# Kernel optimization log

Measured on AMD Instinct MI355X. Metric: run time of the kernel, lower is better.

Reference implementation:

```python
import jax, jax.numpy as jnp
import numpy as np

B, L, T = 32, 256, 32
V_SIZE, D, H = 30000, 300, 256


def _gru(x, h0, Wih, Whh, bih, bhh):
    # x: [B,S,D], h0: [B,H]; PyTorch GRU gate order: r, z, n
    xg = jnp.einsum('bsd,gd->bsg', x, Wih) + bih  # [B,S,3H]

    def step(h, xg_t):
        gh = jnp.einsum('bh,gh->bg', h, Whh) + bhh
        ir, iz, in_ = jnp.split(xg_t, 3, axis=-1)
        hr, hz, hn_ = jnp.split(gh, 3, axis=-1)
        r = jax.nn.sigmoid(ir + hr)
        z = jax.nn.sigmoid(iz + hz)
        n = jnp.tanh(in_ + r * hn_)
        h_new = (1.0 - z) * n + z * h
        return h_new, h_new

    h_last, outs = jax.lax.scan(step, h0, jnp.swapaxes(xg, 0, 1))
    return jnp.swapaxes(outs, 0, 1), h_last  # [B,S,H], [B,H]


def setup_inputs() -> dict:
    rng = np.random.default_rng(0)
    Xin = rng.integers(0, V_SIZE, (B, L)).astype(np.int64)
    # strictly increasing segment ends; starts = previous end + 1
    Yindex = np.stack([np.sort(rng.choice(L, T, replace=False)) for _ in range(B)]).astype(np.int64)
    Xindex = np.concatenate([np.zeros((B, 1), np.int64), Yindex[:, :-1] + 1], axis=1)
    lens = np.full((B,), L, np.int64)
    s = 0.05
    p = lambda *shape: jnp.asarray(rng.standard_normal(shape) * s, jnp.float32)
    return {
        'Xin': jnp.asarray(Xin), 'Xindex': jnp.asarray(Xindex),
        'Yindex': jnp.asarray(Yindex), 'lens': jnp.asarray(lens),
        'emb': jnp.asarray(rng.standard_normal((V_SIZE, D)) * 0.1, jnp.float32),
        'Wih_e': p(3 * H, D), 'Whh_e': p(3 * H, H), 'bih_e': p(3 * H), 'bhh_e': p(3 * H),
        'Wih_d': p(3 * H, D), 'Whh_d': p(3 * H, H), 'bih_d': p(3 * H), 'bhh_d': p(3 * H),
        'W1': p(H, H), 'W2': p(H, H), 'Vv': p(H),
    }


def reference(Xin, Xindex, Yindex, lens, emb, Wih_e, Whh_e, bih_e, bhh_e,
              Wih_d, Whh_d, bih_d, bhh_d, W1, W2, Vv):
    # pointerEncoder (isbanor=False, dropout=0, lens==L so packed == plain)
    X = emb[Xin]                                   # [B,L,D]
    h0 = jnp.zeros((Xin.shape[0], Whh_e.shape[1]), X.dtype)
    hn, h_end = _gru(X, h0, Wih_e, Whh_e, bih_e, bhh_e)  # [B,L,H],[B,H]
    # training_decoder, vectorized over batch and decode steps
    dec_tok = jnp.take_along_axis(Xin, Xindex, axis=1)   # token ids at segment starts
    dx = emb[dec_tok]                              # [B,T,D]
    dout, _ = _gru(dx, h_end, Wih_d, Whh_d, bih_d, bhh_d)  # [B,T,H]
    # pointerLayer: v = selu(V . selu(W1 en + W2 d)), masked log_softmax over [start, curL)
    WE = jnp.einsum('blh,kh->blk', hn, W1)         # [B,L,H]
    WD = jnp.einsum('bth,kh->btk', dout, W2)       # [B,T,H]
    s = jax.nn.selu(WE[:, None, :, :] + WD[:, :, None, :])  # [B,T,L,H]
    v = jax.nn.selu(jnp.einsum('btlh,h->btl', s, Vv))        # [B,T,L]
    pos = jnp.arange(hn.shape[1])
    mask = (pos[None, None, :] >= Xindex[:, :, None]) & (pos[None, None, :] < lens[:, None, None])
    logits = jnp.where(mask, v, -jnp.inf)
    logp = jax.nn.log_softmax(logits, axis=-1)
    tgt_logp = jnp.take_along_axis(logp, Yindex[:, :, None], axis=-1)[..., 0]  # [B,T]
    return -jnp.mean(tgt_logp)  # batch_loss / LoopN
```

## Files before the change

### kernel.cpp

```cpp
#include <hip/hip_runtime.h>
#include <hip/hip_bf16.h>
#include <stdint.h>

#define B_  32
#define L_  256
#define T_  32
#define D_  300
#define H_  256
#define G3  768

__device__ __forceinline__ int sdot4(uint32_t a, uint32_t b, int acc) {
#if defined(__has_builtin) && __has_builtin(__builtin_amdgcn_sdot4)
  return __builtin_amdgcn_sdot4((int)a, (int)b, acc, false);
#else
  const int a0 = (int)(signed char)(a & 0xff),  b0 = (int)(signed char)(b & 0xff);
  const int a1 = (int)(signed char)((a >> 8) & 0xff),  b1 = (int)(signed char)((b >> 8) & 0xff);
  const int a2 = (int)(signed char)((a >> 16) & 0xff), b2 = (int)(signed char)((b >> 16) & 0xff);
  const int a3 = (int)(signed char)(a >> 24),          b3 = (int)(signed char)(b >> 24);
  return acc + a0 * b0 + a1 * b1 + a2 * b2 + a3 * b3;
#endif
}

__device__ __forceinline__ int sdot8(uint32_t a, uint32_t b, int acc) {
#if defined(__has_builtin) && __has_builtin(__builtin_amdgcn_sdot8)
  return __builtin_amdgcn_sdot8((int)a, (int)b, acc, false);
#else
  const uint32_t M = 0xF0F0F0F0u;
  const uint32_t alo = (a << 4) & M, ahi = a & M;
  const uint32_t blo = (b << 4) & M, bhi = b & M;
  return acc + ((sdot4(alo, blo, 0) + sdot4(ahi, bhi, 0)) >> 8);
#endif
}

__device__ __forceinline__ float rcp_f(float x) { return __builtin_amdgcn_rcpf(x); }
__device__ __forceinline__ float sigmoid_f(float x) { return rcp_f(1.0f + __expf(-x)); }
__device__ __forceinline__ float tanh_f(float x) {
  float e2 = __expf(2.0f * x);
  return 1.0f - 2.0f * rcp_f(e2 + 1.0f);
}
__device__ __forceinline__ uint16_t f2bf(float x) {
  uint32_t u = __builtin_bit_cast(uint32_t, x);
  return (uint16_t)((u + 0x7FFF + ((u >> 16) & 1)) >> 16);
}
__device__ __forceinline__ float bf2f(uint16_t b) {
  uint32_t u = ((uint32_t)b) << 16;
  return __builtin_bit_cast(float, u);
}

__device__ __forceinline__ void pack_body(int blk, const float* __restrict__ Whh,
                                          uint32_t* __restrict__ wQ,
                                          float* __restrict__ sw) {
  const int row = blk * 4 + (threadIdx.x >> 6);
  const int lane = threadIdx.x & 63;
  const float* wr = Whh + (long)row * H_;
  float m = 0.0f;
#pragma unroll
  for (int u = 0; u < 4; ++u) m = fmaxf(m, fabsf(wr[lane + 64 * u]));
  for (int off = 32; off > 0; off >>= 1) m = fmaxf(m, __shfl_xor(m, off, 64));
  const float inv = m > 0.0f ? 7.0f / m : 0.0f;
  if (lane == 0) sw[row] = m > 0.0f ? m / 49.0f : 0.0f;
  if (lane < 32) {
    const int pd = lane;
    uint32_t d = 0;
#pragma unroll
    for (int jn = 0; jn < 8; ++jn) {
      int v = __float2int_rn(wr[8 * pd + jn] * inv);
      v = v > 7 ? 7 : (v < -7 ? -7 : v);
      d |= ((uint32_t)(v & 0xF)) << (4 * jn);
    }
    wQ[(((size_t)(pd >> 2) * G3 + row) << 2) + (pd & 3)] = d;
  }
}

__device__ __forceinline__ void quant_body(int blk, const float* __restrict__ A,
                                           const int* __restrict__ rowidx,
                                           const int* __restrict__ Xin2,
                                           const int* __restrict__ Xidx2,
                                           uint32_t* __restrict__ out,
                                           float* __restrict__ scale,
                                           int M, int K, int Kd) {
  const int row = blk * 4 + (threadIdx.x >> 6);
  const int lane = threadIdx.x & 63;
  if (row >= M) return;
  long src = row;
  if (rowidx) src = rowidx[row];
  else if (Xin2) src = Xin2[(row >> 5) * L_ + Xidx2[row]];
  const float* ar = A + src * (long)K;
  float m = 0.0f;
  for (int e = lane; e < K; e += 64) m = fmaxf(m, fabsf(ar[e]));
  for (int off = 32; off > 0; off >>= 1) m = fmaxf(m, __shfl_xor(m, off, 64));
  const float inv = m > 0.0f ? 127.0f / m : 0.0f;
  if (lane == 0) scale[row] = m * (1.0f / 127.0f);
  for (int kd = lane; kd < Kd; kd += 64) {
    uint32_t d = 0;
#pragma unroll
    for (int u = 0; u < 4; ++u) {
      const int e = 4 * kd + u;
      int qv = (e < K) ? __float2int_rn(ar[e] * inv) : 0;
      qv = qv > 127 ? 127 : (qv < -127 ? -127 : qv);
      d |= ((uint32_t)(qv & 0xff)) << (8 * u);
    }
    out[(long)row * Kd + kd] = d;
  }
}

__device__ __forceinline__ void quant16(int blk, const float* __restrict__ A,
                                        uint32_t* __restrict__ out,
                                        float* __restrict__ scale,
                                        int M, int K, int Kd) {
  const int row = blk * 16 + (threadIdx.x >> 6);
  const int lane = threadIdx.x & 63;
  if (row >= M) return;
  const float* ar = A + (long)row * K;
  float m = 0.0f;
  for (int e = lane; e < K; e += 64) m = fmaxf(m, fabsf(ar[e]));
  for (int off = 32; off > 0; off >>= 1) m = fmaxf(m, __shfl_xor(m, off, 64));
  const float inv = m > 0.0f ? 127.0f / m : 0.0f;
  if (lane == 0) scale[row] = m * (1.0f / 127.0f);
  for (int kd = lane; kd < Kd; kd += 64) {
    uint32_t d = 0;
#pragma unroll
    for (int u = 0; u < 4; ++u) {
      const int e = 4 * kd + u;
      int qv = (e < K) ? __float2int_rn(ar[e] * inv) : 0;
      qv = qv > 127 ? 127 : (qv < -127 ? -127 : qv);
      d |= ((uint32_t)(qv & 0xff)) << (8 * u);
    }
    out[(long)row * Kd + kd] = d;
  }
}

__global__ __launch_bounds__(256)
void prep_all(const float* __restrict__ Whh_e, const float* __restrict__ Whh_d,
              uint32_t* __restrict__ wQ_e, uint32_t* __restrict__ wQ_d,
              float* __restrict__ sw_e, float* __restrict__ sw_d,
              const float* __restrict__ Wih_e, const float* __restrict__ Wih_d,
              uint32_t* __restrict__ WihQ_e, uint32_t* __restrict__ WihQ_d,
              float* __restrict__ sWih_e, float* __restrict__ sWih_d,
              const float* __restrict__ W1, const float* __restrict__ W2,
              uint32_t* __restrict__ W1q, uint32_t* __restrict__ W2q,
              float* __restrict__ sW1, float* __restrict__ sW2,
              const float* __restrict__ emb, const int* __restrict__ Xin,
              const int* __restrict__ Xindex,
              uint32_t* __restrict__ Aqe, float* __restrict__ saAe,
              uint32_t* __restrict__ Aqd, float* __restrict__ saAd,
              const float* __restrict__ bih_e, const float* __restrict__ bhh_e,
              float* __restrict__ bsum_e,
              const float* __restrict__ bih_d, const float* __restrict__ bhh_d,
              float* __restrict__ bsum_d) {
  const int blk = blockIdx.x;
  if (blk < 192)        pack_body(blk, Whh_e, wQ_e, sw_e);
  else if (blk < 384)   pack_body(blk - 192, Whh_d, wQ_d, sw_d);
  else if (blk < 576)   quant_body(blk - 384, Wih_e, nullptr, nullptr, nullptr,
                                   WihQ_e, sWih_e, 768, 300, 80);
  else if (blk < 768)   quant_body(blk - 576, Wih_d, nullptr, nullptr, nullptr,
                                   WihQ_d, sWih_d, 768, 300, 80);
  else if (blk < 832)   quant_body(blk - 768, W1, nullptr, nullptr, nullptr,
                                   W1q, sW1, 256, 256, 64);
  else if (blk < 896)   quant_body(blk - 832, W2, nullptr, nullptr, nullptr,
                                   W2q, sW2, 256, 256, 64);
  else if (blk < 2944)  quant_body(blk - 896, emb, Xin, nullptr, nullptr,
                                   Aqe, saAe, 8192, 300, 80);
  else if (blk < 3200)  quant_body(blk - 2944, emb, nullptr, Xin, Xindex,
                                   Aqd, saAd, 1024, 300, 80);
  else {
    const int blk2 = blk - 3200;
    const int i = (blk2 % 3) * 256 + threadIdx.x;
    const float* bih = blk2 < 3 ? bih_e : bih_d;
    const float* bhh = blk2 < 3 ? bhh_e : bhh_d;
    float* bsum = blk2 < 3 ? bsum_e : bsum_d;
    float v = bih[i];
    if (i < 2 * H_) v += bhh[i];
    bsum[i] = v;
  }
}

__device__ __forceinline__
void gemm_body(const uint32_t* __restrict__ Aq, const float* __restrict__ sa,
               const uint32_t* __restrict__ Wq, const float* __restrict__ swc,
               const float* __restrict__ bias, void* __restrict__ C,
               int bm, int bn, int M, int N, int Kd,
               bool transp, bool biasF, bool bf16out) {
  __shared__ uint32_t As[8][68];
  __shared__ uint32_t Ws[8][68];
  const int tid = threadIdx.x;
  const int ty = tid >> 4, tx = tid & 15;
  const int srow = tid >> 2;
  const int skd = (tid & 3) << 1;
  const uint32_t* Arow = Aq + (long)(bm * 64 + srow) * Kd + skd;
  const uint32_t* Wrow = Wq + (long)(bn * 64 + srow) * Kd + skd;
  int acc[4][4] = {};
  for (int k0 = 0; k0 < Kd; k0 += 8) {
    const uint32_t a0 = Arow[k0], a1 = Arow[k0 + 1];
    const uint32_t w0 = Wrow[k0], w1 = Wrow[k0 + 1];
    __syncthreads();
    As[skd][srow] = a0; As[skd + 1][srow] = a1;
    Ws[skd][srow] = w0; Ws[skd + 1][srow] = w1;
    __syncthreads();
#pragma unroll
    for (int kd = 0; kd < 8; ++kd) {
      const uint4 a4 = *(const uint4*)&As[kd][ty << 2];
      const uint4 b4 = *(const uint4*)&Ws[kd][tx << 2];
      acc[0][0] = sdot4(a4.x, b4.x, acc[0][0]);
      acc[0][1] = sdot4(a4.x, b4.y, acc[0][1]);
      acc[0][2] = sdot4(a4.x, b4.z, acc[0][2]);
      acc[0][3] = sdot4(a4.x, b4.w, acc[0][3]);
      acc[1][0] = sdot4(a4.y, b4.x, acc[1][0]);
      acc[1][1] = sdot4(a4.y, b4.y, acc[1][1]);
      acc[1][2] = sdot4(a4.y, b4.z, acc[1][2]);
      acc[1][3] = sdot4(a4.y, b4.w, acc[1][3]);
      acc[2][0] = sdot4(a4.z, b4.x, acc[2][0]);
      acc[2][1] = sdot4(a4.z, b4.y, acc[2][1]);
      acc[2][2] = sdot4(a4.z, b4.z, acc[2][2]);
      acc[2][3] = sdot4(a4.z, b4.w, acc[2][3]);
      acc[3][0] = sdot4(a4.w, b4.x, acc[3][0]);
      acc[3][1] = sdot4(a4.w, b4.y, acc[3][1]);
      acc[3][2] = sdot4(a4.w, b4.z, acc[3][2]);
      acc[3][3] = sdot4(a4.w, b4.w, acc[3][3]);
    }
  }
#pragma unroll
  for (int i = 0; i < 4; ++i) {
    const int m = bm * 64 + (ty << 2) + i;
    const float sai = sa[m];
#pragma unroll
    for (int j = 0; j < 4; ++j) {
      const int n = bn * 64 + (tx << 2) + j;
      float v = (float)acc[i][j] * sai * swc[n];
      if (biasF) v += bias[n];
      const long idx = transp ? ((((long)(m >> 8) * N + n) << 8) + (m & 255))
                              : ((long)m * N + n);
      if (bf16out) ((uint16_t*)C)[idx] = f2bf(v);
      else         ((float*)C)[idx] = v;
    }
  }
}

__global__ __launch_bounds__(256)
void xg_gemms(const uint32_t* __restrict__ Aqe, const float* __restrict__ saAe,
              const uint32_t* __restrict__ WihQ_e, const float* __restrict__ sWih_e,
              const float* __restrict__ bsum_e, uint16_t* __restrict__ xg_e,
              const uint32_t* __restrict__ Aqd, const float* __restrict__ saAd,
              const uint32_t* __restrict__ WihQ_d, const float* __restrict__ sWih_d,
              const float* __restrict__ bsum_d, uint16_t* __restrict__ xg_d) {
  const int blk = blockIdx.x;
  if (blk < 1536)
    gemm_body(Aqe, saAe, WihQ_e, sWih_e, bsum_e, xg_e,
              blk % 128, blk / 128, 8192, 768, 80, false, true, true);
  else {
    const int k = blk - 1536;
    gemm_body(Aqd, saAd, WihQ_d, sWih_d, bsum_d, xg_d,
              k % 16, k / 16, 1024, 768, 80, false, true, true);
  }
}


#define PIN4(v) asm volatile("" : "+v"(v.x), "+v"(v.y), "+v"(v.z), "+v"(v.w))
#define DOT8V(acc, p_, h_) { \
  acc = sdot8(p_.x, h_.x, acc); acc = sdot8(p_.y, h_.y, acc); \
  acc = sdot8(p_.z, h_.z, acc); acc = sdot8(p_.w, h_.w, acc); }

#define LGKM_BARRIER() { \
  asm volatile("s_waitcnt lgkmcnt(0)" ::: "memory"); \
  __builtin_amdgcn_s_barrier(); }

__device__ __forceinline__
void gru_block(int b, const uint16_t* __restrict__ xg, const uint4* __restrict__ wQv,
               const float* __restrict__ sw, const float* __restrict__ bhh,
               const float* __restrict__ h0, float* __restrict__ hout,
               float* __restrict__ hlast, int S,
               uint32_t (*h2)[32], int4 (*partv)[H_]) {
  const int tid = threadIdx.x;
  const int j = tid & 255;
  const int q = tid >> 8;
  const uint4* wp = wQv + (q * 2) * G3 + j;
  uint4 wr0 = wp[0],      wr1 = wp[G3];
  uint4 wz0 = wp[H_],     wz1 = wp[G3 + H_];
  uint4 wn0 = wp[2 * H_], wn1 = wp[G3 + 2 * H_];
  PIN4(wr0); PIN4(wr1); PIN4(wz0); PIN4(wz1); PIN4(wn0); PIN4(wn1);
  float bhn = 0.0f, h = 0.0f, swr = 0.0f, swz = 0.0f, swn = 0.0f;
  const uint16_t* xp = xg + (long)b * S * G3;
  float* hp_out = hout + (long)b * S * H_;
  if (q == 0) {
    bhn = bhh[2 * H_ + j];
    swr = sw[j]; swz = sw[H_ + j]; swn = sw[2 * H_ + j];
    h = h0 ? h0[b * H_ + j] : 0.0f;
    int hq4 = __float2int_rn(h * 7.0f);
    hq4 = hq4 > 7 ? 7 : (hq4 < -7 ? -7 : hq4);
    const int hq4n = __shfl_down(hq4, 1, 64);
    if (!(j & 1))
      ((uint8_t*)h2[0])[j >> 1] = (uint8_t)((hq4 & 0xF) | ((hq4n & 0xF) << 4));
  }
  __syncthreads();
  for (int t = 0; t < S; ++t) {
    const uint4* hq = (const uint4*)h2[t & 1] + q * 2;
    const uint4 ha = hq[0], hb = hq[1];
    float xr = 0.0f, xz = 0.0f, xn = 0.0f;
    if (q == 0) {
      xr = bf2f(xp[j]); xz = bf2f(xp[H_ + j]); xn = bf2f(xp[2 * H_ + j]);
    }
    int ar = 0, az = 0, an = 0;
    DOT8V(ar, wr0, ha) DOT8V(ar, wr1, hb)
    DOT8V(az, wz0, ha) DOT8V(az, wz1, hb)
    DOT8V(an, wn0, ha) DOT8V(an, wn1, hb)
    if (q) partv[q][j] = make_int4(ar, az, an, 0);
    LGKM_BARRIER();
    if (q == 0) {
      const int4 p1 = partv[1][j];
      const int4 p2 = partv[2][j];
      const int4 p3 = partv[3][j];
      const float arf = (float)(ar + p1.x + p2.x + p3.x) * swr;
      const float azf = (float)(az + p1.y + p2.y + p3.y) * swz;
      const float anf = (float)(an + p1.z + p2.z + p3.z) * swn;
      const float r = sigmoid_f(xr + arf);
      const float z = sigmoid_f(xz + azf);
      const float n = tanh_f(xn + r * (anf + bhn));
      h = (1.0f - z) * n + z * h;
      hp_out[j] = h;
      int hq4 = __float2int_rn(h * 7.0f);
      hq4 = hq4 > 7 ? 7 : (hq4 < -7 ? -7 : hq4);
      const int hq4n = __shfl_down(hq4, 1, 64);
      if (!(j & 1))
        ((uint8_t*)h2[(t & 1) ^ 1])[j >> 1] =
            (uint8_t)((hq4 & 0xF) | ((hq4n & 0xF) << 4));
    }
    xp += G3;
    hp_out += H_;
    LGKM_BARRIER();
  }
  if (q == 0 && hlast) hlast[b * H_ + j] = h;
}

__global__ __launch_bounds__(1024)
void gru_enc(const uint16_t* __restrict__ xg, const uint4* __restrict__ wQv,
             const float* __restrict__ sw, const float* __restrict__ bhh,
             float* __restrict__ hout, float* __restrict__ hlast, int S) {
  __shared__ __align__(16) uint32_t h2[2][32];
  __shared__ int4 partv[4][H_];
  gru_block(blockIdx.x, xg, wQv, sw, bhh, nullptr, hout, hlast, S, h2, partv);
}

__global__ __launch_bounds__(1024)
void dec_and_hquant(const uint16_t* __restrict__ xg_d, const uint4* __restrict__ wQ_d,
                    const float* __restrict__ sw_d, const float* __restrict__ bhh_d,
                    const float* __restrict__ hend, float* __restrict__ doutb,
                    const float* __restrict__ hn, uint32_t* __restrict__ hnq,
                    float* __restrict__ sahn) {
  __shared__ __align__(16) uint32_t h2[2][32];
  __shared__ int4 partv[4][H_];
  if (blockIdx.x < 32)
    gru_block(blockIdx.x, xg_d, wQ_d, sw_d, bhh_d, hend, doutb,
              (float*)nullptr, T_, h2, partv);
  else
    quant16(blockIdx.x - 32, hn, hnq, sahn, 8192, 256, 64);
}

__global__ __launch_bounds__(256)
void wet_and_dquant(const uint32_t* __restrict__ hnq, const float* __restrict__ sahn,
                    const uint32_t* __restrict__ W1q, const float* __restrict__ sW1,
                    float* __restrict__ WEt,
                    const float* __restrict__ doutb, uint32_t* __restrict__ dq,
                    float* __restrict__ sad) {
  if (blockIdx.x < 512)
    gemm_body(hnq, sahn, W1q, sW1, nullptr, WEt,
              blockIdx.x & 127, blockIdx.x >> 7, 8192, 256, 64, true, false, false);
  else
    quant_body(blockIdx.x - 512, doutb, nullptr, nullptr, nullptr,
               dq, sad, 1024, 256, 64);
}

__global__ __launch_bounds__(256)
void wd_gemm(const uint32_t* __restrict__ dq, const float* __restrict__ sad,
             const uint32_t* __restrict__ W2q, const float* __restrict__ sW2,
             float* __restrict__ WDb) {
  gemm_body(dq, sad, W2q, sW2, nullptr, WDb,
            blockIdx.x & 15, blockIdx.x >> 4, 1024, 256, 64, false, false, false);
}

__global__ __launch_bounds__(256)
void pointer_loss(const float* __restrict__ WEt, const float* __restrict__ WD,
                  const float* __restrict__ Vv,
                  const int* __restrict__ Xindex, const int* __restrict__ Yindex,
                  const int* __restrict__ lens, float* __restrict__ out) {
  const int t = blockIdx.x, b = blockIdx.y;
  const int l = threadIdx.x;
  __shared__ float wd_s[H_], vv_s[H_];
  __shared__ float rbuf[4], sbuf[4], vy_s;
  const int bt = b * T_ + t;
  wd_s[l] = WD[(long)bt * H_ + l];
  vv_s[l] = Vv[l] * 1.0507009873554805f;
  __syncthreads();
  const float* wet = WEt + (long)b * H_ * L_;
  const float alpha = 1.6732632423543772f;
  float acc = 0.0f;
#pragma unroll 4
  for (int hh = 0; hh < H_; ++hh) {
    const float xsum = wet[hh * L_ + l] + wd_s[hh];
    const float sneg = alpha * (__expf(xsum) - 1.0f);
    const float s = xsum > 0.0f ? xsum : sneg;
    acc = fmaf(s, vv_s[hh], acc);
  }
  float v;
  {
    const float sneg = alpha * (__expf(acc) - 1.0f);
    v = 1.0507009873554805f * (acc > 0.0f ? acc : sneg);
  }
  const int start = Xindex[bt];
  const int len = lens[b];
  const bool valid = (l >= start) && (l < len);
  const int y = Yindex[bt];
  if (l == y) vy_s = v;
  float m = valid ? v : -INFINITY;
  for (int off = 32; off > 0; off >>= 1) m = fmaxf(m, __shfl_xor(m, off, 64));
  const int wid = l >> 6, lane = l & 63;
  if (lane == 0) rbuf[wid] = m;
  __syncthreads();
  const float mx = fmaxf(fmaxf(rbuf[0], rbuf[1]), fmaxf(rbuf[2], rbuf[3]));
  float e = valid ? __expf(v - mx) : 0.0f;
  for (int off = 32; off > 0; off >>= 1) e += __shfl_xor(e, off, 64);
  if (lane == 0) sbuf[wid] = e;
  __syncthreads();
  if (l == 0) {
    const float sum = sbuf[0] + sbuf[1] + sbuf[2] + sbuf[3];
    atomicAdd(out, (mx + __logf(sum) - vy_s) * (1.0f / (B_ * T_)));
  }
}

extern "C" void kernel_launch(void* const* d_in, const int* in_sizes, int n_in,
                              void* d_out, int out_size, void* d_ws, size_t ws_size,
                              hipStream_t stream) {
  (void)in_sizes; (void)n_in; (void)out_size; (void)ws_size;
  const int*   Xin    = (const int*)d_in[0];
  const int*   Xindex = (const int*)d_in[1];
  const int*   Yindex = (const int*)d_in[2];
  const int*   lens   = (const int*)d_in[3];
  const float* emb    = (const float*)d_in[4];
  const float* Wih_e  = (const float*)d_in[5];
  const float* Whh_e  = (const float*)d_in[6];
  const float* bih_e  = (const float*)d_in[7];
  const float* bhh_e  = (const float*)d_in[8];
  const float* Wih_d  = (const float*)d_in[9];
  const float* Whh_d  = (const float*)d_in[10];
  const float* bih_d  = (const float*)d_in[11];
  const float* bhh_d  = (const float*)d_in[12];
  const float* W1     = (const float*)d_in[13];
  const float* W2     = (const float*)d_in[14];
  const float* Vv     = (const float*)d_in[15];

  char* p = (char*)d_ws;
  auto take = [&](size_t bytes) { void* q = (void*)p; p += (bytes + 255) & ~(size_t)255; return q; };
  uint32_t* wQ_e   = (uint32_t*)take((size_t)32 * G3 * 4);
  uint32_t* wQ_d   = (uint32_t*)take((size_t)32 * G3 * 4);
  float*    sw_e   = (float*)take((size_t)768 * 4);
  float*    sw_d   = (float*)take((size_t)768 * 4);
  uint32_t* WihQ_e = (uint32_t*)take((size_t)768 * 80 * 4);
  uint32_t* WihQ_d = (uint32_t*)take((size_t)768 * 80 * 4);
  float*    sWih_e = (float*)take((size_t)768 * 4);
  float*    sWih_d = (float*)take((size_t)768 * 4);
  uint32_t* W1q    = (uint32_t*)take((size_t)256 * 64 * 4);
  uint32_t* W2q    = (uint32_t*)take((size_t)256 * 64 * 4);
  float*    sW1    = (float*)take((size_t)256 * 4);
  float*    sW2    = (float*)take((size_t)256 * 4);
  float*    bsum_e = (float*)take((size_t)768 * 4);
  float*    bsum_d = (float*)take((size_t)768 * 4);
  uint16_t* xg_e   = (uint16_t*)take((size_t)8192 * 768 * 2);
  uint16_t* xg_d   = (uint16_t*)take((size_t)1024 * 768 * 2);
  float*    hn     = (float*)take((size_t)8192 * 256 * 4);
  float*    hend   = (float*)take((size_t)8192 * 4);
  float*    doutb  = (float*)take((size_t)1024 * 256 * 4);
  float*    WDb    = (float*)take((size_t)1024 * 256 * 4);
  float*    WEt    = (float*)take((size_t)8192 * 256 * 4);
  uint32_t* Aqe    = (uint32_t*)take((size_t)8192 * 80 * 4);
  float*    saAe   = (float*)take((size_t)8192 * 4);
  uint32_t* Aqd    = (uint32_t*)take((size_t)1024 * 80 * 4);
  float*    saAd   = (float*)take((size_t)1024 * 4);
  uint32_t* hnq  = Aqe;
  float*    sahn = saAe;
  uint32_t* dq   = Aqd;
  float*    sad  = saAd;

  hipMemsetAsync(d_out, 0, sizeof(float), stream);

  hipLaunchKernelGGL(prep_all, dim3(3206), dim3(256), 0, stream,
                     Whh_e, Whh_d, wQ_e, wQ_d, sw_e, sw_d,
                     Wih_e, Wih_d, WihQ_e, WihQ_d, sWih_e, sWih_d,
                     W1, W2, W1q, W2q, sW1, sW2,
                     emb, Xin, Xindex, Aqe, saAe, Aqd, saAd,
                     bih_e, bhh_e, bsum_e, bih_d, bhh_d, bsum_d);

  hipLaunchKernelGGL(xg_gemms, dim3(1728), dim3(256), 0, stream,
                     Aqe, saAe, WihQ_e, sWih_e, bsum_e, xg_e,
                     Aqd, saAd, WihQ_d, sWih_d, bsum_d, xg_d);

  hipLaunchKernelGGL(gru_enc, dim3(32), dim3(1024), 0, stream,
                     xg_e, (const uint4*)wQ_e, sw_e, bhh_e, hn, hend, L_);

  hipLaunchKernelGGL(dec_and_hquant, dim3(544), dim3(1024), 0, stream,
                     xg_d, (const uint4*)wQ_d, sw_d, bhh_d, hend, doutb,
                     hn, hnq, sahn);

  hipLaunchKernelGGL(wet_and_dquant, dim3(768), dim3(256), 0, stream,
                     hnq, sahn, W1q, sW1, WEt, doutb, dq, sad);

  hipLaunchKernelGGL(wd_gemm, dim3(64), dim3(256), 0, stream,
                     dq, sad, W2q, sW2, WDb);

  hipLaunchKernelGGL(pointer_loss, dim3(T_, B_), dim3(256), 0, stream,
                     WEt, WDb, Vv, Xindex, Yindex, lens, (float*)d_out);
}
```

Before: 287.2 us.

## Run GRU recurrence with one thread per hidden unit, dropping cross-wave reduction

Each GRU block now uses 256 threads, and each thread holds the full recurrent weight row (96 uint4 registers) for its hidden unit. This removes the 4-way K split, the LDS partial-sum exchange and one barrier per timestep. It also prefetches the next step's input gates into registers so the global load overlaps the dot products. The cost is much higher register pressure and fewer waves per block to hide latency. The hn quantization blocks move to 4-row 256-thread blocks, which raises their grid count.

```diff
diff --git a/kernel.cpp b/kernel.cpp
--- a/kernel.cpp
+++ b/kernel.cpp
@@ -86,32 +86,6 @@
   if (rowidx) src = rowidx[row];
   else if (Xin2) src = Xin2[(row >> 5) * L_ + Xidx2[row]];
   const float* ar = A + src * (long)K;
-  float m = 0.0f;
-  for (int e = lane; e < K; e += 64) m = fmaxf(m, fabsf(ar[e]));
-  for (int off = 32; off > 0; off >>= 1) m = fmaxf(m, __shfl_xor(m, off, 64));
-  const float inv = m > 0.0f ? 127.0f / m : 0.0f;
-  if (lane == 0) scale[row] = m * (1.0f / 127.0f);
-  for (int kd = lane; kd < Kd; kd += 64) {
-    uint32_t d = 0;
-#pragma unroll
-    for (int u = 0; u < 4; ++u) {
-      const int e = 4 * kd + u;
-      int qv = (e < K) ? __float2int_rn(ar[e] * inv) : 0;
-      qv = qv > 127 ? 127 : (qv < -127 ? -127 : qv);
-      d |= ((uint32_t)(qv & 0xff)) << (8 * u);
-    }
-    out[(long)row * Kd + kd] = d;
-  }
-}
-
-__device__ __forceinline__ void quant16(int blk, const float* __restrict__ A,
-                                        uint32_t* __restrict__ out,
-                                        float* __restrict__ scale,
-                                        int M, int K, int Kd) {
-  const int row = blk * 16 + (threadIdx.x >> 6);
-  const int lane = threadIdx.x & 63;
-  if (row >= M) return;
-  const float* ar = A + (long)row * K;
   float m = 0.0f;
   for (int e = lane; e < K; e += 64) m = fmaxf(m, fabsf(ar[e]));
   for (int off = 32; off > 0; off >>= 1) m = fmaxf(m, __shfl_xor(m, off, 64));
@@ -264,95 +238,99 @@
   asm volatile("s_waitcnt lgkmcnt(0)" ::: "memory"); \
   __builtin_amdgcn_s_barrier(); }
 
+#define CHUNK(c) { \
+  const uint4 hc = hq[c]; \
+  DOT8V(ar, wr##c, hc) DOT8V(az, wz##c, hc) DOT8V(an, wn##c, hc) }
+
 __device__ __forceinline__
 void gru_block(int b, const uint16_t* __restrict__ xg, const uint4* __restrict__ wQv,
                const float* __restrict__ sw, const float* __restrict__ bhh,
                const float* __restrict__ h0, float* __restrict__ hout,
-               float* __restrict__ hlast, int S,
-               uint32_t (*h2)[32], int4 (*partv)[H_]) {
-  const int tid = threadIdx.x;
-  const int j = tid & 255;
-  const int q = tid >> 8;
-  const uint4* wp = wQv + (q * 2) * G3 + j;
-  uint4 wr0 = wp[0],      wr1 = wp[G3];
-  uint4 wz0 = wp[H_],     wz1 = wp[G3 + H_];
-  uint4 wn0 = wp[2 * H_], wn1 = wp[G3 + 2 * H_];
-  PIN4(wr0); PIN4(wr1); PIN4(wz0); PIN4(wz1); PIN4(wn0); PIN4(wn1);
-  float bhn = 0.0f, h = 0.0f, swr = 0.0f, swz = 0.0f, swn = 0.0f;
-  const uint16_t* xp = xg + (long)b * S * G3;
-  float* hp_out = hout + (long)b * S * H_;
-  if (q == 0) {
-    bhn = bhh[2 * H_ + j];
-    swr = sw[j]; swz = sw[H_ + j]; swn = sw[2 * H_ + j];
-    h = h0 ? h0[b * H_ + j] : 0.0f;
+               float* __restrict__ hlast, int S, uint32_t (*h2)[32]) {
+  const int j = threadIdx.x;
+  uint4 wr0 = wQv[0 * G3 + j],      wr1 = wQv[1 * G3 + j];
+  uint4 wr2 = wQv[2 * G3 + j],      wr3 = wQv[3 * G3 + j];
+  uint4 wr4 = wQv[4 * G3 + j],      wr5 = wQv[5 * G3 + j];
+  uint4 wr6 = wQv[6 * G3 + j],      wr7 = wQv[7 * G3 + j];
+  uint4 wz0 = wQv[0 * G3 + H_ + j], wz1 = wQv[1 * G3 + H_ + j];
+  uint4 wz2 = wQv[2 * G3 + H_ + j], wz3 = wQv[3 * G3 + H_ + j];
+  uint4 wz4 = wQv[4 * G3 + H_ + j], wz5 = wQv[5 * G3 + H_ + j];
+  uint4 wz6 = wQv[6 * G3 + H_ + j], wz7 = wQv[7 * G3 + H_ + j];
+  uint4 wn0 = wQv[0 * G3 + 2 * H_ + j], wn1 = wQv[1 * G3 + 2 * H_ + j];
+  uint4 wn2 = wQv[2 * G3 + 2 * H_ + j], wn3 = wQv[3 * G3 + 2 * H_ + j];
+  uint4 wn4 = wQv[4 * G3 + 2 * H_ + j], wn5 = wQv[5 * G3 + 2 * H_ + j];
+  uint4 wn6 = wQv[6 * G3 + 2 * H_ + j], wn7 = wQv[7 * G3 + 2 * H_ + j];
+  PIN4(wr0); PIN4(wr1); PIN4(wr2); PIN4(wr3);
+  PIN4(wr4); PIN4(wr5); PIN4(wr6); PIN4(wr7);
+  PIN4(wz0); PIN4(wz1); PIN4(wz2); PIN4(wz3);
+  PIN4(wz4); PIN4(wz5); PIN4(wz6); PIN4(wz7);
+  PIN4(wn0); PIN4(wn1); PIN4(wn2); PIN4(wn3);
+  PIN4(wn4); PIN4(wn5); PIN4(wn6); PIN4(wn7);
+  const float bhn = bhh[2 * H_ + j];
+  const float swr = sw[j], swz = sw[H_ + j], swn = sw[2 * H_ + j];
+  float h = h0 ? h0[b * H_ + j] : 0.0f;
+  {
     int hq4 = __float2int_rn(h * 7.0f);
     hq4 = hq4 > 7 ? 7 : (hq4 < -7 ? -7 : hq4);
     const int hq4n = __shfl_down(hq4, 1, 64);
     if (!(j & 1))
       ((uint8_t*)h2[0])[j >> 1] = (uint8_t)((hq4 & 0xF) | ((hq4n & 0xF) << 4));
   }
+  const uint16_t* xp = xg + (long)b * S * G3;
+  float* hp_out = hout + (long)b * S * H_;
+  float xr = bf2f(xp[j]), xz = bf2f(xp[H_ + j]), xn = bf2f(xp[2 * H_ + j]);
   __syncthreads();
   for (int t = 0; t < S; ++t) {
-    const uint4* hq = (const uint4*)h2[t & 1] + q * 2;
-    const uint4 ha = hq[0], hb = hq[1];
-    float xr = 0.0f, xz = 0.0f, xn = 0.0f;
-    if (q == 0) {
-      xr = bf2f(xp[j]); xz = bf2f(xp[H_ + j]); xn = bf2f(xp[2 * H_ + j]);
+    float nxr = 0.0f, nxz = 0.0f, nxn = 0.0f;
+    if (t + 1 < S) {
+      nxr = bf2f(xp[G3 + j]);
+      nxz = bf2f(xp[G3 + H_ + j]);
+      nxn = bf2f(xp[G3 + 2 * H_ + j]);
     }
+    const uint4* hq = (const uint4*)h2[t & 1];
     int ar = 0, az = 0, an = 0;
-    DOT8V(ar, wr0, ha) DOT8V(ar, wr1, hb)
-    DOT8V(az, wz0, ha) DOT8V(az, wz1, hb)
-    DOT8V(an, wn0, ha) DOT8V(an, wn1, hb)
-    if (q) partv[q][j] = make_int4(ar, az, an, 0);
-    LGKM_BARRIER();
-    if (q == 0) {
-      const int4 p1 = partv[1][j];
-      const int4 p2 = partv[2][j];
-      const int4 p3 = partv[3][j];
-      const float arf = (float)(ar + p1.x + p2.x + p3.x) * swr;
-      const float azf = (float)(az + p1.y + p2.y + p3.y) * swz;
-      const float anf = (float)(an + p1.z + p2.z + p3.z) * swn;
-      const float r = sigmoid_f(xr + arf);
-      const float z = sigmoid_f(xz + azf);
-      const float n = tanh_f(xn + r * (anf + bhn));
-      h = (1.0f - z) * n + z * h;
-      hp_out[j] = h;
-      int hq4 = __float2int_rn(h * 7.0f);
-      hq4 = hq4 > 7 ? 7 : (hq4 < -7 ? -7 : hq4);
-      const int hq4n = __shfl_down(hq4, 1, 64);
-      if (!(j & 1))
-        ((uint8_t*)h2[(t & 1) ^ 1])[j >> 1] =
-            (uint8_t)((hq4 & 0xF) | ((hq4n & 0xF) << 4));
-    }
+    CHUNK(0) CHUNK(1) CHUNK(2) CHUNK(3)
+    CHUNK(4) CHUNK(5) CHUNK(6) CHUNK(7)
+    const float r = sigmoid_f(xr + (float)ar * swr);
+    const float z = sigmoid_f(xz + (float)az * swz);
+    const float n = tanh_f(xn + r * ((float)an * swn + bhn));
+    h = (1.0f - z) * n + z * h;
+    hp_out[j] = h;
+    int hq4 = __float2int_rn(h * 7.0f);
+    hq4 = hq4 > 7 ? 7 : (hq4 < -7 ? -7 : hq4);
+    const int hq4n = __shfl_down(hq4, 1, 64);
+    if (!(j & 1))
+      ((uint8_t*)h2[(t & 1) ^ 1])[j >> 1] =
+          (uint8_t)((hq4 & 0xF) | ((hq4n & 0xF) << 4));
+    xr = nxr; xz = nxz; xn = nxn;
     xp += G3;
     hp_out += H_;
     LGKM_BARRIER();
   }
-  if (q == 0 && hlast) hlast[b * H_ + j] = h;
-}
-
-__global__ __launch_bounds__(1024)
+  if (hlast) hlast[b * H_ + j] = h;
+}
+
+__global__ __launch_bounds__(256)
 void gru_enc(const uint16_t* __restrict__ xg, const uint4* __restrict__ wQv,
              const float* __restrict__ sw, const float* __restrict__ bhh,
              float* __restrict__ hout, float* __restrict__ hlast, int S) {
   __shared__ __align__(16) uint32_t h2[2][32];
-  __shared__ int4 partv[4][H_];
-  gru_block(blockIdx.x, xg, wQv, sw, bhh, nullptr, hout, hlast, S, h2, partv);
-}
-
-__global__ __launch_bounds__(1024)
+  gru_block(blockIdx.x, xg, wQv, sw, bhh, nullptr, hout, hlast, S, h2);
+}
+
+__global__ __launch_bounds__(256)
 void dec_and_hquant(const uint16_t* __restrict__ xg_d, const uint4* __restrict__ wQ_d,
                     const float* __restrict__ sw_d, const float* __restrict__ bhh_d,
                     const float* __restrict__ hend, float* __restrict__ doutb,
                     const float* __restrict__ hn, uint32_t* __restrict__ hnq,
                     float* __restrict__ sahn) {
   __shared__ __align__(16) uint32_t h2[2][32];
-  __shared__ int4 partv[4][H_];
   if (blockIdx.x < 32)
     gru_block(blockIdx.x, xg_d, wQ_d, sw_d, bhh_d, hend, doutb,
-              (float*)nullptr, T_, h2, partv);
+              (float*)nullptr, T_, h2);
   else
-    quant16(blockIdx.x - 32, hn, hnq, sahn, 8192, 256, 64);
+    quant_body(blockIdx.x - 32, hn, nullptr, nullptr, nullptr,
+               hnq, sahn, 8192, 256, 64);
 }
 
 __global__ __launch_bounds__(256)
@@ -492,10 +470,10 @@
                      Aqe, saAe, WihQ_e, sWih_e, bsum_e, xg_e,
                      Aqd, saAd, WihQ_d, sWih_d, bsum_d, xg_d);
 
-  hipLaunchKernelGGL(gru_enc, dim3(32), dim3(1024), 0, stream,
+  hipLaunchKernelGGL(gru_enc, dim3(32), dim3(256), 0, stream,
                      xg_e, (const uint4*)wQ_e, sw_e, bhh_e, hn, hend, L_);
 
-  hipLaunchKernelGGL(dec_and_hquant, dim3(544), dim3(1024), 0, stream,
+  hipLaunchKernelGGL(dec_and_hquant, dim3(2080), dim3(256), 0, stream,
                      xg_d, (const uint4*)wQ_d, sw_d, bhh_d, hend, doutb,
                      hn, hnq, sahn);
 
```

Result: slower. 327.8 us (+14.1%).
